# Kernel tuning notes

Hardware: AMD Instinct MI355X
Metric: run time of the kernel (lower is better)

The kernel has to match this reference:

```python
import jax, jax.numpy as jnp
import numpy as np

VOCAB_SIZE = 126
N_LABELS = VOCAB_SIZE + 2  # 128
START_IDX = N_LABELS - 2
STOP_IDX = N_LABELS - 1
NEG_INF = -10000.0


def setup_inputs() -> dict:
    key = jax.random.key(0)
    k1, k2, k3 = jax.random.split(key, 3)
    B, T = 512, 512
    logits = jax.random.normal(k1, (B, T, N_LABELS), dtype=jnp.float32)
    lens = jax.random.randint(k2, (B,), 1, T + 1, dtype=jnp.int64)
    transitions = jax.random.normal(k3, (N_LABELS, N_LABELS), dtype=jnp.float32)
    # CRF constraints from __init__: nothing transitions FROM start-as-target row,
    # nothing transitions INTO stop column (transitions[i, j] = score j -> i).
    transitions = transitions.at[START_IDX, :].set(NEG_INF)
    transitions = transitions.at[:, STOP_IDX].set(NEG_INF)
    return {"logits": logits, "lens": lens, "transitions": transitions}


def reference(logits, lens, transitions):
    """CRF forward algorithm (log partition function). Returns [B] norm."""
    B, T, n = logits.shape
    alpha0 = jnp.full((B, n), NEG_INF, dtype=logits.dtype).at[:, START_IDX].set(0.0)
    # mask[t, b] = 1 while t < lens[b] (matches c_lens > 0 per-step update)
    mask = (jnp.arange(T)[:, None] < lens[None, :]).astype(logits.dtype)  # [T, B]
    logits_t = jnp.transpose(logits, (1, 0, 2))  # [T, B, n]

    def step(alpha, inp):
        logit, m = inp  # [B, n], [B]
        # alpha_nxt[b, i] = logit[b, i] + logsumexp_j(trans[i, j] + alpha[b, j])
        alpha_nxt = jax.nn.logsumexp(transitions[None, :, :] + alpha[:, None, :], axis=2) + logit
        m = m[:, None]
        alpha = m * alpha_nxt + (1.0 - m) * alpha
        return alpha, None

    alpha, _ = jax.lax.scan(step, alpha0, (logits_t, mask))
    alpha = alpha + transitions[STOP_IDX][None, :]
    return jax.nn.logsumexp(alpha, axis=1)  # [B]
```

## Files before the change

### kernel.cpp

```cpp
#include <hip/hip_runtime.h>

#define NL 128
#define TT 512
#define NB 512
#define START_IDX 126
#define STOP_IDX 127

typedef __attribute__((ext_vector_type(8))) short bf16x8;
typedef __attribute__((ext_vector_type(4))) float f32x4;
typedef __attribute__((ext_vector_type(4))) unsigned u32x4;

__device__ __forceinline__ short f2bf(float x) {
    union { float f; unsigned u; } v; v.f = x;
    unsigned r = (v.u + 0x7FFFu + ((v.u >> 16) & 1u)) >> 16;
    return (short)r;
}

__device__ __forceinline__ unsigned cvt_pk_bf16(float lo, float hi) {
    unsigned r;
    asm("v_cvt_pk_bf16_f32 %0, %1, %2" : "=v"(r) : "v"(lo), "v"(hi));
    return r;
}

#define BAR() do {                                                            \
    asm volatile("s_waitcnt lgkmcnt(0)" ::: "memory");                        \
    __builtin_amdgcn_s_barrier();                                             \
} while (0)

#define MFMA16(A_, B_, C_) __builtin_amdgcn_mfma_f32_16x16x32_bf16(A_, B_, C_, 0, 0, 0)

#define STEP(T_, PUB_, CONS_, EU_, EB_, RS_, RD_) do {                        \
    u32x4 bo_ = {bw0, bw1, bw2, bw3};                                         \
    bf16x8 bO_ = __builtin_bit_cast(bf16x8, bo_);                             \
    bf16x8 bA_ = __builtin_bit_cast(bf16x8, bvA);                             \
    bf16x8 bB_ = __builtin_bit_cast(bf16x8, bvB);                             \
    bf16x8 bC_ = __builtin_bit_cast(bf16x8, bvC);                             \
    f32x4 a0_ = {0.f,0.f,0.f,0.f}, a1_ = {0.f,0.f,0.f,0.f};                   \
    a0_ = MFMA16(afr[0][0], bO_, a0_);                                        \
    a1_ = MFMA16(afr[1][0], bO_, a1_);                                        \
    a0_ = MFMA16(afr[0][1], bA_, a0_);                                        \
    a1_ = MFMA16(afr[1][1], bA_, a1_);                                        \
    a0_ = MFMA16(afr[0][2], bB_, a0_);                                        \
    a1_ = MFMA16(afr[1][2], bB_, a1_);                                        \
    a0_ = MFMA16(afr[0][3], bC_, a0_);                                        \
    a1_ = MFMA16(afr[1][3], bC_, a1_);                                        \
    { int tp_ = (T_) + 3; if (tp_ > TT - 1) tp_ = TT - 1;                     \
      const float* lp_ = lsrc + (size_t)tp_ * NL;                             \
      RD_##A = *(const f32x4*)(lp_ + eo0);                                    \
      RD_##B = *(const f32x4*)(lp_ + eo1); }                                  \
    _Pragma("unroll")                                                         \
    for (int r_ = 0; r_ < 4; ++r_) {                                          \
        EB_##A[r_] = __expf(RS_##A[r_]);                                      \
        EB_##B[r_] = __expf(RS_##B[r_]);                                      \
    }                                                                         \
    float nv0_[4], nv1_[4];                                                   \
    _Pragma("unroll")                                                         \
    for (int r_ = 0; r_ < 4; ++r_) {                                          \
        nv0_[r_] = a0_[r_] * EU_##A[r_];                                      \
        nv1_[r_] = a1_[r_] * EU_##B[r_];                                      \
    }                                                                         \
    const bool live_ = (T_) < lenc;                                           \
    if (CONS_) {                                                              \
        float mx_ = fmaxf(fmaxf(smax[0][c], smax[1][c]),                      \
                          fmaxf(smax[2][c], smax[3][c]));                     \
        const unsigned eb_ = (__float_as_uint(mx_) >> 23) & 0xFFu;            \
        const float sc_ = __uint_as_float(((253u - eb_) & 0xFFu) << 23);      \
        _Pragma("unroll")                                                     \
        for (int r_ = 0; r_ < 4; ++r_) { nv0_[r_] *= sc_; nv1_[r_] *= sc_; }  \
        if (live_) cbi += (int)eb_ - 126;                                     \
    }                                                                         \
    if (PUB_) {                                                               \
        float lm_ = fmaxf(fmaxf(fmaxf(nv0_[0], nv0_[1]), fmaxf(nv0_[2], nv0_[3])), \
                          fmaxf(fmaxf(nv1_[0], nv1_[1]), fmaxf(nv1_[2], nv1_[3]))); \
        lm_ = fmaxf(lm_, __shfl_xor(lm_, 16));                                \
        lm_ = fmaxf(lm_, __shfl_xor(lm_, 32));                                \
        if (g == 0) smax[w][c] = lm_;                                         \
    }                                                                         \
    { const unsigned n0_ = cvt_pk_bf16(nv0_[0], nv0_[1]);                     \
      const unsigned n1_ = cvt_pk_bf16(nv0_[2], nv0_[3]);                     \
      const unsigned n2_ = cvt_pk_bf16(nv1_[0], nv1_[1]);                     \
      const unsigned n3_ = cvt_pk_bf16(nv1_[2], nv1_[3]);                     \
      bw0 = live_ ? n0_ : bw0;  bw1 = live_ ? n1_ : bw1;                      \
      bw2 = live_ ? n2_ : bw2;  bw3 = live_ ? n3_ : bw3; }                    \
    char* nb_ = sb[((T_) + 1) & 1];                                           \
    { u32x4 wv_ = {bw0, bw1, bw2, bw3};                                       \
      *(u32x4*)(nb_ + w * 1280 + slotOff) = wv_; }                            \
    BAR();                                                                    \
    bvA = *(const u32x4*)(nb_ + kA + slotOff);                                \
    bvB = *(const u32x4*)(nb_ + kB + slotOff);                                \
    bvC = *(const u32x4*)(nb_ + kC + slotOff);                                \
} while (0)

__global__ __launch_bounds__(256)
void crf_scan(const float* __restrict__ logits,
              const int* __restrict__ lens,
              const float* __restrict__ trans,
              float* __restrict__ out)
{
    const int b0   = blockIdx.x * 16;
    const int tid  = threadIdx.x;
    const int w    = tid >> 6;
    const int lane = tid & 63;
    const int c    = lane & 15;
    const int g    = lane >> 4;

    __shared__ __align__(16) char sb[2][4 * 16 * 80];
    __shared__ float smax[4][16];

    bf16x8 afr[2][4];
    #pragma unroll
    for (int mi = 0; mi < 2; ++mi) {
        const int M = w + 4 * mi;
        const float* rowp = trans + (M * 16 + c) * NL + 4 * g;
        #pragma unroll
        for (int pos = 0; pos < 4; ++pos) {
            const int kk = (w + pos) & 3;
            f32x4 lo4 = *(const f32x4*)(rowp + kk * 16);
            f32x4 hi4 = *(const f32x4*)(rowp + (kk + 4) * 16);
            bf16x8 a;
            #pragma unroll
            for (int j = 0; j < 4; ++j) {
                a[j]     = f2bf(__expf(lo4[j]));
                a[j + 4] = f2bf(__expf(hi4[j]));
            }
            afr[mi][pos] = a;
        }
    }

    int lenc = lens[b0 + c];
    lenc = lenc < 1 ? 1 : (lenc > TT ? TT : lenc);
    int gl = lenc;
    #pragma unroll
    for (int d = 1; d < 16; d <<= 1) { int o = __shfl_xor(gl, d); gl = gl > o ? gl : o; }
    const int glen = __builtin_amdgcn_readfirstlane(gl);

    const int slotOff = c * 80 + g * 16;
    const int kA = ((w + 1) & 3) * 1280;
    const int kB = ((w + 2) & 3) * 1280;
    const int kC = ((w + 3) & 3) * 1280;

    unsigned bw0 = 0u, bw1 = 0u, bw2 = 0u,
             bw3 = (w == 3 && g == 3) ? 0x00003F80u : 0u;
    { u32x4 z = {bw0, bw1, bw2, bw3};
      *(u32x4*)(sb[0] + w * 1280 + slotOff) = z; }
    BAR();
    u32x4 bvA = *(const u32x4*)(sb[0] + kA + slotOff);
    u32x4 bvB = *(const u32x4*)(sb[0] + kB + slotOff);
    u32x4 bvC = *(const u32x4*)(sb[0] + kC + slotOff);

    const float* lsrc = logits + (size_t)(b0 + c) * TT * NL;
    const int eo0 = w * 16 + 4 * g;
    const int eo1 = (w + 4) * 16 + 4 * g;

    f32x4 R0A, R0B, R1A, R1B, R2A, R2B, R3A, R3B;
    f32x4 E0A, E0B, E1A, E1B;
    R0A = *(const f32x4*)(lsrc + eo0);            R0B = *(const f32x4*)(lsrc + eo1);
    R1A = *(const f32x4*)(lsrc + NL + eo0);       R1B = *(const f32x4*)(lsrc + NL + eo1);
    R2A = *(const f32x4*)(lsrc + 2 * NL + eo0);   R2B = *(const f32x4*)(lsrc + 2 * NL + eo1);
    #pragma unroll
    for (int r = 0; r < 4; ++r) {
        E0A[r] = __expf(R0A[r]);  E0B[r] = __expf(R0B[r]);
    }

    int cbi = 0;
    int t = 0;
    const int tmain = glen & ~3;
    for (; t < tmain; t += 4) {
        STEP(t + 0, false, false, E0, E1, R1, R3);
        STEP(t + 1, false, false, E1, E0, R2, R0);
        STEP(t + 2, true,  false, E0, E1, R3, R1);
        STEP(t + 3, false, true,  E1, E0, R0, R2);
    }
    if (t < glen) { STEP(t, false, false, E0, E1, R1, R3); ++t; }
    if (t < glen) { STEP(t, false, false, E1, E0, R2, R0); ++t; }
    if (t < glen) { STEP(t, true,  false, E0, E1, R3, R1); ++t; }

    if (w == 0) {
        float s = 0.f;
        const float* stopr = trans + STOP_IDX * NL + 4 * g;
        u32x4 grp[4];
        grp[0] = (u32x4){bw0, bw1, bw2, bw3};
        grp[1] = bvA; grp[2] = bvB; grp[3] = bvC;
        #pragma unroll
        for (int kk = 0; kk < 4; ++kk) {
            f32x4 t0 = *(const f32x4*)(stopr + kk * 16);
            f32x4 t1 = *(const f32x4*)(stopr + (kk + 4) * 16);
            #pragma unroll
            for (int i = 0; i < 2; ++i) {
                const unsigned wd = grp[kk][i];
                s += __uint_as_float(wd << 16)         * __expf(t0[2 * i]);
                s += __uint_as_float(wd & 0xFFFF0000u) * __expf(t0[2 * i + 1]);
            }
            #pragma unroll
            for (int i = 2; i < 4; ++i) {
                const unsigned wd = grp[kk][i];
                s += __uint_as_float(wd << 16)         * __expf(t1[2 * (i - 2)]);
                s += __uint_as_float(wd & 0xFFFF0000u) * __expf(t1[2 * (i - 2) + 1]);
            }
        }
        s += __shfl_xor(s, 16);
        s += __shfl_xor(s, 32);
        if (g == 0)
            out[b0 + c] = (float)cbi * 0.69314718055994531f + __logf(s);
    }
}

extern "C" void kernel_launch(void* const* d_in, const int* in_sizes, int n_in,
                              void* d_out, int out_size, void* d_ws, size_t ws_size,
                              hipStream_t stream) {
    const float* logits = (const float*)d_in[0];
    const int*   lens   = (const int*)d_in[1];
    const float* trans  = (const float*)d_in[2];
    float*       outp   = (float*)d_out;
    crf_scan<<<NB / 16, 256, 0, stream>>>(logits, lens, trans, outp);
}
```

Baseline: 150.6 us.

## Interleave two independent batch groups per block to hide scan-step latency

Each block now processes two 16-sequence groups (32 sequences) with duplicated register state, shared-memory buffers and max slots. The two groups' steps are interleaved so that one barrier per step serves both chains, and the MFMA and exp latency of one chain can overlap the other. The grid is halved to 16 blocks, so fewer CUs are in use. Each block also runs to the longest length among 32 sequences instead of 16, and register pressure roughly doubles.

```diff
diff --git a/kernel.cpp b/kernel.cpp
--- a/kernel.cpp
+++ b/kernel.cpp
@@ -29,83 +29,123 @@
 
 #define MFMA16(A_, B_, C_) __builtin_amdgcn_mfma_f32_16x16x32_bf16(A_, B_, C_, 0, 0, 0)
 
-#define STEP(T_, PUB_, CONS_, EU_, EB_, RS_, RD_) do {                        \
-    u32x4 bo_ = {bw0, bw1, bw2, bw3};                                         \
+#define STEP_PRE(P, PI_, T_, PUB_, CONS_, EU_, EB_, RS_, RD_) do {            \
+    u32x4 bo_ = {P##_bw0, P##_bw1, P##_bw2, P##_bw3};                         \
     bf16x8 bO_ = __builtin_bit_cast(bf16x8, bo_);                             \
-    bf16x8 bA_ = __builtin_bit_cast(bf16x8, bvA);                             \
-    bf16x8 bB_ = __builtin_bit_cast(bf16x8, bvB);                             \
-    bf16x8 bC_ = __builtin_bit_cast(bf16x8, bvC);                             \
+    bf16x8 bA_ = __builtin_bit_cast(bf16x8, P##_bvA);                         \
+    bf16x8 bB_ = __builtin_bit_cast(bf16x8, P##_bvB);                         \
+    bf16x8 bC_ = __builtin_bit_cast(bf16x8, P##_bvC);                         \
     f32x4 a0_ = {0.f,0.f,0.f,0.f}, a1_ = {0.f,0.f,0.f,0.f};                   \
-    a0_ = MFMA16(afr[0][0], bO_, a0_);                                        \
-    a1_ = MFMA16(afr[1][0], bO_, a1_);                                        \
-    a0_ = MFMA16(afr[0][1], bA_, a0_);                                        \
-    a1_ = MFMA16(afr[1][1], bA_, a1_);                                        \
-    a0_ = MFMA16(afr[0][2], bB_, a0_);                                        \
-    a1_ = MFMA16(afr[1][2], bB_, a1_);                                        \
-    a0_ = MFMA16(afr[0][3], bC_, a0_);                                        \
-    a1_ = MFMA16(afr[1][3], bC_, a1_);                                        \
+    a0_ = MFMA16(afr[0][0], bO_, a0_);  a1_ = MFMA16(afr[1][0], bO_, a1_);    \
+    a0_ = MFMA16(afr[0][1], bA_, a0_);  a1_ = MFMA16(afr[1][1], bA_, a1_);    \
+    a0_ = MFMA16(afr[0][2], bB_, a0_);  a1_ = MFMA16(afr[1][2], bB_, a1_);    \
+    a0_ = MFMA16(afr[0][3], bC_, a0_);  a1_ = MFMA16(afr[1][3], bC_, a1_);    \
     { int tp_ = (T_) + 3; if (tp_ > TT - 1) tp_ = TT - 1;                     \
-      const float* lp_ = lsrc + (size_t)tp_ * NL;                             \
-      RD_##A = *(const f32x4*)(lp_ + eo0);                                    \
-      RD_##B = *(const f32x4*)(lp_ + eo1); }                                  \
+      const float* lp_ = P##_lsrc + (size_t)tp_ * NL;                         \
+      P##_##RD_##X = *(const f32x4*)(lp_ + eo0);                              \
+      P##_##RD_##Y = *(const f32x4*)(lp_ + eo1); }                            \
     _Pragma("unroll")                                                         \
     for (int r_ = 0; r_ < 4; ++r_) {                                          \
-        EB_##A[r_] = __expf(RS_##A[r_]);                                      \
-        EB_##B[r_] = __expf(RS_##B[r_]);                                      \
+        P##_##EB_##X[r_] = __expf(P##_##RS_##X[r_]);                          \
+        P##_##EB_##Y[r_] = __expf(P##_##RS_##Y[r_]);                          \
     }                                                                         \
     float nv0_[4], nv1_[4];                                                   \
     _Pragma("unroll")                                                         \
     for (int r_ = 0; r_ < 4; ++r_) {                                          \
-        nv0_[r_] = a0_[r_] * EU_##A[r_];                                      \
-        nv1_[r_] = a1_[r_] * EU_##B[r_];                                      \
-    }                                                                         \
-    const bool live_ = (T_) < lenc;                                           \
+        nv0_[r_] = a0_[r_] * P##_##EU_##X[r_];                                \
+        nv1_[r_] = a1_[r_] * P##_##EU_##Y[r_];                                \
+    }                                                                         \
+    const bool live_ = (T_) < P##_lenc;                                       \
     if (CONS_) {                                                              \
-        float mx_ = fmaxf(fmaxf(smax[0][c], smax[1][c]),                      \
-                          fmaxf(smax[2][c], smax[3][c]));                     \
+        float mx_ = fmaxf(fmaxf(sm##P[0][c], sm##P[1][c]),                    \
+                          fmaxf(sm##P[2][c], sm##P[3][c]));                   \
         const unsigned eb_ = (__float_as_uint(mx_) >> 23) & 0xFFu;            \
         const float sc_ = __uint_as_float(((253u - eb_) & 0xFFu) << 23);      \
         _Pragma("unroll")                                                     \
         for (int r_ = 0; r_ < 4; ++r_) { nv0_[r_] *= sc_; nv1_[r_] *= sc_; }  \
-        if (live_) cbi += (int)eb_ - 126;                                     \
+        if (live_) P##_cbi += (int)eb_ - 126;                                 \
     }                                                                         \
     if (PUB_) {                                                               \
         float lm_ = fmaxf(fmaxf(fmaxf(nv0_[0], nv0_[1]), fmaxf(nv0_[2], nv0_[3])), \
                           fmaxf(fmaxf(nv1_[0], nv1_[1]), fmaxf(nv1_[2], nv1_[3]))); \
         lm_ = fmaxf(lm_, __shfl_xor(lm_, 16));                                \
         lm_ = fmaxf(lm_, __shfl_xor(lm_, 32));                                \
-        if (g == 0) smax[w][c] = lm_;                                         \
+        if (g == 0) sm##P[w][c] = lm_;                                        \
     }                                                                         \
     { const unsigned n0_ = cvt_pk_bf16(nv0_[0], nv0_[1]);                     \
       const unsigned n1_ = cvt_pk_bf16(nv0_[2], nv0_[3]);                     \
       const unsigned n2_ = cvt_pk_bf16(nv1_[0], nv1_[1]);                     \
       const unsigned n3_ = cvt_pk_bf16(nv1_[2], nv1_[3]);                     \
-      bw0 = live_ ? n0_ : bw0;  bw1 = live_ ? n1_ : bw1;                      \
-      bw2 = live_ ? n2_ : bw2;  bw3 = live_ ? n3_ : bw3; }                    \
-    char* nb_ = sb[((T_) + 1) & 1];                                           \
-    { u32x4 wv_ = {bw0, bw1, bw2, bw3};                                       \
-      *(u32x4*)(nb_ + w * 1280 + slotOff) = wv_; }                            \
+      P##_bw0 = live_ ? n0_ : P##_bw0;  P##_bw1 = live_ ? n1_ : P##_bw1;      \
+      P##_bw2 = live_ ? n2_ : P##_bw2;  P##_bw3 = live_ ? n3_ : P##_bw3; }    \
+    { u32x4 wv_ = {P##_bw0, P##_bw1, P##_bw2, P##_bw3};                       \
+      *(u32x4*)(&sb[PI_][((T_) + 1) & 1][0] + w * 1280 + slotOff) = wv_; }    \
+} while (0)
+
+#define STEP_POST(P, PI_, T_) do {                                            \
+    const char* nb_ = &sb[PI_][((T_) + 1) & 1][0];                            \
+    P##_bvA = *(const u32x4*)(nb_ + kA + slotOff);                            \
+    P##_bvB = *(const u32x4*)(nb_ + kB + slotOff);                            \
+    P##_bvC = *(const u32x4*)(nb_ + kC + slotOff);                            \
+} while (0)
+
+#define ROUND(T_, PUB_, CONS_, EU_, EB_, RS_, RD_) do {                       \
+    STEP_PRE(A, 0, T_, PUB_, CONS_, EU_, EB_, RS_, RD_);                      \
+    STEP_PRE(B, 1, T_, PUB_, CONS_, EU_, EB_, RS_, RD_);                      \
     BAR();                                                                    \
-    bvA = *(const u32x4*)(nb_ + kA + slotOff);                                \
-    bvB = *(const u32x4*)(nb_ + kB + slotOff);                                \
-    bvC = *(const u32x4*)(nb_ + kC + slotOff);                                \
-} while (0)
-
-__global__ __launch_bounds__(256)
+    STEP_POST(A, 0, T_);                                                      \
+    STEP_POST(B, 1, T_);                                                      \
+} while (0)
+
+#define EPILOG(P, BB_) do {                                                   \
+    float s = 0.f;                                                            \
+    const float* stopr = trans + STOP_IDX * NL + 4 * g;                       \
+    _Pragma("unroll")                                                         \
+    for (int pos = 0; pos < 4; ++pos) {                                       \
+        const int kk = (w + pos) & 3;                                         \
+        u32x4 gv;                                                             \
+        if (pos == 0)      gv = (u32x4){P##_bw0, P##_bw1, P##_bw2, P##_bw3};  \
+        else if (pos == 1) gv = P##_bvA;                                      \
+        else if (pos == 2) gv = P##_bvB;                                      \
+        else               gv = P##_bvC;                                      \
+        f32x4 t0 = *(const f32x4*)(stopr + kk * 16);                          \
+        f32x4 t1 = *(const f32x4*)(stopr + (kk + 4) * 16);                    \
+        _Pragma("unroll")                                                     \
+        for (int i = 0; i < 2; ++i) {                                         \
+            const unsigned wd = gv[i];                                        \
+            s += __uint_as_float(wd << 16)         * __expf(t0[2 * i]);       \
+            s += __uint_as_float(wd & 0xFFFF0000u) * __expf(t0[2 * i + 1]);   \
+        }                                                                     \
+        _Pragma("unroll")                                                     \
+        for (int i = 2; i < 4; ++i) {                                         \
+            const unsigned wd = gv[i];                                        \
+            s += __uint_as_float(wd << 16)         * __expf(t1[2 * (i - 2)]); \
+            s += __uint_as_float(wd & 0xFFFF0000u) * __expf(t1[2 * (i - 2) + 1]); \
+        }                                                                     \
+    }                                                                         \
+    s += __shfl_xor(s, 16);                                                   \
+    s += __shfl_xor(s, 32);                                                   \
+    if (g == 0)                                                               \
+        out[(BB_) + c] = (float)P##_cbi * 0.69314718055994531f + __logf(s);   \
+} while (0)
+
+__global__ __launch_bounds__(256, 1)
 void crf_scan(const float* __restrict__ logits,
               const int* __restrict__ lens,
               const float* __restrict__ trans,
               float* __restrict__ out)
 {
-    const int b0   = blockIdx.x * 16;
+    const int b0A  = blockIdx.x * 32;
+    const int b0B  = b0A + 16;
     const int tid  = threadIdx.x;
     const int w    = tid >> 6;
     const int lane = tid & 63;
     const int c    = lane & 15;
     const int g    = lane >> 4;
 
-    __shared__ __align__(16) char sb[2][4 * 16 * 80];
-    __shared__ float smax[4][16];
+    __shared__ __align__(16) char sb[2][2][4 * 16 * 80];
+    __shared__ float smA[4][16];
+    __shared__ float smB[4][16];
 
     bf16x8 afr[2][4];
     #pragma unroll
@@ -127,9 +167,11 @@
         }
     }
 
-    int lenc = lens[b0 + c];
-    lenc = lenc < 1 ? 1 : (lenc > TT ? TT : lenc);
-    int gl = lenc;
+    int A_lenc = lens[b0A + c];
+    A_lenc = A_lenc < 1 ? 1 : (A_lenc > TT ? TT : A_lenc);
+    int B_lenc = lens[b0B + c];
+    B_lenc = B_lenc < 1 ? 1 : (B_lenc > TT ? TT : B_lenc);
+    int gl = A_lenc > B_lenc ? A_lenc : B_lenc;
     #pragma unroll
     for (int d = 1; d < 16; d <<= 1) { int o = __shfl_xor(gl, d); gl = gl > o ? gl : o; }
     const int glen = __builtin_amdgcn_readfirstlane(gl);
@@ -139,70 +181,56 @@
     const int kB = ((w + 2) & 3) * 1280;
     const int kC = ((w + 3) & 3) * 1280;
 
-    unsigned bw0 = 0u, bw1 = 0u, bw2 = 0u,
-             bw3 = (w == 3 && g == 3) ? 0x00003F80u : 0u;
-    { u32x4 z = {bw0, bw1, bw2, bw3};
-      *(u32x4*)(sb[0] + w * 1280 + slotOff) = z; }
+    unsigned A_bw0 = 0u, A_bw1 = 0u, A_bw2 = 0u,
+             A_bw3 = (w == 3 && g == 3) ? 0x00003F80u : 0u;
+    unsigned B_bw0 = 0u, B_bw1 = 0u, B_bw2 = 0u, B_bw3 = A_bw3;
+    { u32x4 z = {A_bw0, A_bw1, A_bw2, A_bw3};
+      *(u32x4*)(&sb[0][0][0] + w * 1280 + slotOff) = z;
+      *(u32x4*)(&sb[1][0][0] + w * 1280 + slotOff) = z; }
     BAR();
-    u32x4 bvA = *(const u32x4*)(sb[0] + kA + slotOff);
-    u32x4 bvB = *(const u32x4*)(sb[0] + kB + slotOff);
-    u32x4 bvC = *(const u32x4*)(sb[0] + kC + slotOff);
-
-    const float* lsrc = logits + (size_t)(b0 + c) * TT * NL;
+    u32x4 A_bvA = *(const u32x4*)(&sb[0][0][0] + kA + slotOff);
+    u32x4 A_bvB = *(const u32x4*)(&sb[0][0][0] + kB + slotOff);
+    u32x4 A_bvC = *(const u32x4*)(&sb[0][0][0] + kC + slotOff);
+    u32x4 B_bvA = *(const u32x4*)(&sb[1][0][0] + kA + slotOff);
+    u32x4 B_bvB = *(const u32x4*)(&sb[1][0][0] + kB + slotOff);
+    u32x4 B_bvC = *(const u32x4*)(&sb[1][0][0] + kC + slotOff);
+
+    const float* A_lsrc = logits + (size_t)(b0A + c) * TT * NL;
+    const float* B_lsrc = logits + (size_t)(b0B + c) * TT * NL;
     const int eo0 = w * 16 + 4 * g;
     const int eo1 = (w + 4) * 16 + 4 * g;
 
-    f32x4 R0A, R0B, R1A, R1B, R2A, R2B, R3A, R3B;
-    f32x4 E0A, E0B, E1A, E1B;
-    R0A = *(const f32x4*)(lsrc + eo0);            R0B = *(const f32x4*)(lsrc + eo1);
-    R1A = *(const f32x4*)(lsrc + NL + eo0);       R1B = *(const f32x4*)(lsrc + NL + eo1);
-    R2A = *(const f32x4*)(lsrc + 2 * NL + eo0);   R2B = *(const f32x4*)(lsrc + 2 * NL + eo1);
+    f32x4 A_R0X, A_R0Y, A_R1X, A_R1Y, A_R2X, A_R2Y, A_R3X, A_R3Y;
+    f32x4 A_E0X, A_E0Y, A_E1X, A_E1Y;
+    f32x4 B_R0X, B_R0Y, B_R1X, B_R1Y, B_R2X, B_R2Y, B_R3X, B_R3Y;
+    f32x4 B_E0X, B_E0Y, B_E1X, B_E1Y;
+    A_R0X = *(const f32x4*)(A_lsrc + eo0);          A_R0Y = *(const f32x4*)(A_lsrc + eo1);
+    A_R1X = *(const f32x4*)(A_lsrc + NL + eo0);     A_R1Y = *(const f32x4*)(A_lsrc + NL + eo1);
+    A_R2X = *(const f32x4*)(A_lsrc + 2 * NL + eo0); A_R2Y = *(const f32x4*)(A_lsrc + 2 * NL + eo1);
+    B_R0X = *(const f32x4*)(B_lsrc + eo0);          B_R0Y = *(const f32x4*)(B_lsrc + eo1);
+    B_R1X = *(const f32x4*)(B_lsrc + NL + eo0);     B_R1Y = *(const f32x4*)(B_lsrc + NL + eo1);
+    B_R2X = *(const f32x4*)(B_lsrc + 2 * NL + eo0); B_R2Y = *(const f32x4*)(B_lsrc + 2 * NL + eo1);
     #pragma unroll
     for (int r = 0; r < 4; ++r) {
-        E0A[r] = __expf(R0A[r]);  E0B[r] = __expf(R0B[r]);
+        A_E0X[r] = __expf(A_R0X[r]);  A_E0Y[r] = __expf(A_R0Y[r]);
+        B_E0X[r] = __expf(B_R0X[r]);  B_E0Y[r] = __expf(B_R0Y[r]);
     }
 
-    int cbi = 0;
+    int A_cbi = 0, B_cbi = 0;
     int t = 0;
     const int tmain = glen & ~3;
     for (; t < tmain; t += 4) {
-        STEP(t + 0, false, false, E0, E1, R1, R3);
-        STEP(t + 1, false, false, E1, E0, R2, R0);
-        STEP(t + 2, true,  false, E0, E1, R3, R1);
-        STEP(t + 3, false, true,  E1, E0, R0, R2);
+        ROUND(t + 0, false, false, E0, E1, R1, R3);
+        ROUND(t + 1, false, false, E1, E0, R2, R0);
+        ROUND(t + 2, true,  false, E0, E1, R3, R1);
+        ROUND(t + 3, false, true,  E1, E0, R0, R2);
     }
-    if (t < glen) { STEP(t, false, false, E0, E1, R1, R3); ++t; }
-    if (t < glen) { STEP(t, false, false, E1, E0, R2, R0); ++t; }
-    if (t < glen) { STEP(t, true,  false, E0, E1, R3, R1); ++t; }
-
-    if (w == 0) {
-        float s = 0.f;
-        const float* stopr = trans + STOP_IDX * NL + 4 * g;
-        u32x4 grp[4];
-        grp[0] = (u32x4){bw0, bw1, bw2, bw3};
-        grp[1] = bvA; grp[2] = bvB; grp[3] = bvC;
-        #pragma unroll
-        for (int kk = 0; kk < 4; ++kk) {
-            f32x4 t0 = *(const f32x4*)(stopr + kk * 16);
-            f32x4 t1 = *(const f32x4*)(stopr + (kk + 4) * 16);
-            #pragma unroll
-            for (int i = 0; i < 2; ++i) {
-                const unsigned wd = grp[kk][i];
-                s += __uint_as_float(wd << 16)         * __expf(t0[2 * i]);
-                s += __uint_as_float(wd & 0xFFFF0000u) * __expf(t0[2 * i + 1]);
-            }
-            #pragma unroll
-            for (int i = 2; i < 4; ++i) {
-                const unsigned wd = grp[kk][i];
-                s += __uint_as_float(wd << 16)         * __expf(t1[2 * (i - 2)]);
-                s += __uint_as_float(wd & 0xFFFF0000u) * __expf(t1[2 * (i - 2) + 1]);
-            }
-        }
-        s += __shfl_xor(s, 16);
-        s += __shfl_xor(s, 32);
-        if (g == 0)
-            out[b0 + c] = (float)cbi * 0.69314718055994531f + __logf(s);
-    }
+    if (t < glen) { ROUND(t, false, false, E0, E1, R1, R3); ++t; }
+    if (t < glen) { ROUND(t, false, false, E1, E0, R2, R0); ++t; }
+    if (t < glen) { ROUND(t, true,  false, E0, E1, R3, R1); ++t; }
+
+    if (w == 0)      EPILOG(A, b0A);
+    else if (w == 1) EPILOG(B, b0B);
 }
 
 extern "C" void kernel_launch(void* const* d_in, const int* in_sizes, int n_in,
@@ -212,5 +240,5 @@
     const int*   lens   = (const int*)d_in[1];
     const float* trans  = (const float*)d_in[2];
     float*       outp   = (float*)d_out;
-    crf_scan<<<NB / 16, 256, 0, stream>>>(logits, lens, trans, outp);
-}
+    crf_scan<<<NB / 32, 256, 0, stream>>>(logits, lens, trans, outp);
+}
```

Result: slower. 251.9 us (+67.2%).

## Halve workgroup to two waves, each computing four output tiles per step

Applied to the files above, without the earlier changes.

Each block now runs 2 wavefronts instead of 4. Each wave computes 64 of the 128 output labels per step with 16 MFMAs, and the transition-matrix fragments held per wave double. The goal is to cut the per-step barrier and LDS exchange cost and the cross-wave max reduction in the serial recurrence. In exchange each wave does twice the MFMA and exp work per step, carries more registers, and the grid still has only 32 blocks, so per-step latency may grow.

```diff
diff --git a/kernel.cpp b/kernel.cpp
--- a/kernel.cpp
+++ b/kernel.cpp
@@ -30,68 +30,87 @@
 #define MFMA16(A_, B_, C_) __builtin_amdgcn_mfma_f32_16x16x32_bf16(A_, B_, C_, 0, 0, 0)
 
 #define STEP(T_, PUB_, CONS_, EU_, EB_, RS_, RD_) do {                        \
-    u32x4 bo_ = {bw0, bw1, bw2, bw3};                                         \
-    bf16x8 bO_ = __builtin_bit_cast(bf16x8, bo_);                             \
-    bf16x8 bA_ = __builtin_bit_cast(bf16x8, bvA);                             \
-    bf16x8 bB_ = __builtin_bit_cast(bf16x8, bvB);                             \
-    bf16x8 bC_ = __builtin_bit_cast(bf16x8, bvC);                             \
+    u32x4 bp_ = {bwP0, bwP1, bwP2, bwP3};                                     \
+    u32x4 bq_ = {bwQ0, bwQ1, bwQ2, bwQ3};                                     \
+    bf16x8 bP_ = __builtin_bit_cast(bf16x8, bp_);                             \
+    bf16x8 bQ_ = __builtin_bit_cast(bf16x8, bq_);                             \
+    bf16x8 bX_ = __builtin_bit_cast(bf16x8, bvX);                             \
+    bf16x8 bY_ = __builtin_bit_cast(bf16x8, bvY);                             \
     f32x4 a0_ = {0.f,0.f,0.f,0.f}, a1_ = {0.f,0.f,0.f,0.f};                   \
-    a0_ = MFMA16(afr[0][0], bO_, a0_);                                        \
-    a1_ = MFMA16(afr[1][0], bO_, a1_);                                        \
-    a0_ = MFMA16(afr[0][1], bA_, a0_);                                        \
-    a1_ = MFMA16(afr[1][1], bA_, a1_);                                        \
-    a0_ = MFMA16(afr[0][2], bB_, a0_);                                        \
-    a1_ = MFMA16(afr[1][2], bB_, a1_);                                        \
-    a0_ = MFMA16(afr[0][3], bC_, a0_);                                        \
-    a1_ = MFMA16(afr[1][3], bC_, a1_);                                        \
+    f32x4 a2_ = {0.f,0.f,0.f,0.f}, a3_ = {0.f,0.f,0.f,0.f};                   \
+    a0_ = MFMA16(afr[0][0], bP_, a0_);  a1_ = MFMA16(afr[1][0], bP_, a1_);    \
+    a2_ = MFMA16(afr[2][0], bP_, a2_);  a3_ = MFMA16(afr[3][0], bP_, a3_);    \
+    a0_ = MFMA16(afr[0][1], bQ_, a0_);  a1_ = MFMA16(afr[1][1], bQ_, a1_);    \
+    a2_ = MFMA16(afr[2][1], bQ_, a2_);  a3_ = MFMA16(afr[3][1], bQ_, a3_);    \
+    a0_ = MFMA16(afr[0][2], bX_, a0_);  a1_ = MFMA16(afr[1][2], bX_, a1_);    \
+    a2_ = MFMA16(afr[2][2], bX_, a2_);  a3_ = MFMA16(afr[3][2], bX_, a3_);    \
+    a0_ = MFMA16(afr[0][3], bY_, a0_);  a1_ = MFMA16(afr[1][3], bY_, a1_);    \
+    a2_ = MFMA16(afr[2][3], bY_, a2_);  a3_ = MFMA16(afr[3][3], bY_, a3_);    \
     { int tp_ = (T_) + 3; if (tp_ > TT - 1) tp_ = TT - 1;                     \
       const float* lp_ = lsrc + (size_t)tp_ * NL;                             \
-      RD_##A = *(const f32x4*)(lp_ + eo0);                                    \
-      RD_##B = *(const f32x4*)(lp_ + eo1); }                                  \
+      RD_##A = *(const f32x4*)(lp_ + eoA);                                    \
+      RD_##B = *(const f32x4*)(lp_ + eoB);                                    \
+      RD_##C = *(const f32x4*)(lp_ + eoC);                                    \
+      RD_##D = *(const f32x4*)(lp_ + eoD); }                                  \
     _Pragma("unroll")                                                         \
     for (int r_ = 0; r_ < 4; ++r_) {                                          \
         EB_##A[r_] = __expf(RS_##A[r_]);                                      \
         EB_##B[r_] = __expf(RS_##B[r_]);                                      \
-    }                                                                         \
-    float nv0_[4], nv1_[4];                                                   \
+        EB_##C[r_] = __expf(RS_##C[r_]);                                      \
+        EB_##D[r_] = __expf(RS_##D[r_]);                                      \
+    }                                                                         \
+    float nv0_[4], nv1_[4], nv2_[4], nv3_[4];                                 \
     _Pragma("unroll")                                                         \
     for (int r_ = 0; r_ < 4; ++r_) {                                          \
         nv0_[r_] = a0_[r_] * EU_##A[r_];                                      \
         nv1_[r_] = a1_[r_] * EU_##B[r_];                                      \
+        nv2_[r_] = a2_[r_] * EU_##C[r_];                                      \
+        nv3_[r_] = a3_[r_] * EU_##D[r_];                                      \
     }                                                                         \
     const bool live_ = (T_) < lenc;                                           \
     if (CONS_) {                                                              \
-        float mx_ = fmaxf(fmaxf(smax[0][c], smax[1][c]),                      \
-                          fmaxf(smax[2][c], smax[3][c]));                     \
+        float mx_ = fmaxf(smax[0][c], smax[1][c]);                            \
         const unsigned eb_ = (__float_as_uint(mx_) >> 23) & 0xFFu;            \
         const float sc_ = __uint_as_float(((253u - eb_) & 0xFFu) << 23);      \
         _Pragma("unroll")                                                     \
-        for (int r_ = 0; r_ < 4; ++r_) { nv0_[r_] *= sc_; nv1_[r_] *= sc_; }  \
+        for (int r_ = 0; r_ < 4; ++r_) {                                      \
+            nv0_[r_] *= sc_; nv1_[r_] *= sc_;                                 \
+            nv2_[r_] *= sc_; nv3_[r_] *= sc_;                                 \
+        }                                                                     \
         if (live_) cbi += (int)eb_ - 126;                                     \
     }                                                                         \
     if (PUB_) {                                                               \
         float lm_ = fmaxf(fmaxf(fmaxf(nv0_[0], nv0_[1]), fmaxf(nv0_[2], nv0_[3])), \
                           fmaxf(fmaxf(nv1_[0], nv1_[1]), fmaxf(nv1_[2], nv1_[3]))); \
+        lm_ = fmaxf(lm_, fmaxf(fmaxf(nv2_[0], nv2_[1]), fmaxf(nv2_[2], nv2_[3]))); \
+        lm_ = fmaxf(lm_, fmaxf(fmaxf(nv3_[0], nv3_[1]), fmaxf(nv3_[2], nv3_[3]))); \
         lm_ = fmaxf(lm_, __shfl_xor(lm_, 16));                                \
         lm_ = fmaxf(lm_, __shfl_xor(lm_, 32));                                \
         if (g == 0) smax[w][c] = lm_;                                         \
     }                                                                         \
-    { const unsigned n0_ = cvt_pk_bf16(nv0_[0], nv0_[1]);                     \
-      const unsigned n1_ = cvt_pk_bf16(nv0_[2], nv0_[3]);                     \
-      const unsigned n2_ = cvt_pk_bf16(nv1_[0], nv1_[1]);                     \
-      const unsigned n3_ = cvt_pk_bf16(nv1_[2], nv1_[3]);                     \
-      bw0 = live_ ? n0_ : bw0;  bw1 = live_ ? n1_ : bw1;                      \
-      bw2 = live_ ? n2_ : bw2;  bw3 = live_ ? n3_ : bw3; }                    \
+    { const unsigned p0_ = cvt_pk_bf16(nv0_[0], nv0_[1]);                     \
+      const unsigned p1_ = cvt_pk_bf16(nv0_[2], nv0_[3]);                     \
+      const unsigned p2_ = cvt_pk_bf16(nv2_[0], nv2_[1]);                     \
+      const unsigned p3_ = cvt_pk_bf16(nv2_[2], nv2_[3]);                     \
+      const unsigned q0_ = cvt_pk_bf16(nv1_[0], nv1_[1]);                     \
+      const unsigned q1_ = cvt_pk_bf16(nv1_[2], nv1_[3]);                     \
+      const unsigned q2_ = cvt_pk_bf16(nv3_[0], nv3_[1]);                     \
+      const unsigned q3_ = cvt_pk_bf16(nv3_[2], nv3_[3]);                     \
+      bwP0 = live_ ? p0_ : bwP0;  bwP1 = live_ ? p1_ : bwP1;                  \
+      bwP2 = live_ ? p2_ : bwP2;  bwP3 = live_ ? p3_ : bwP3;                  \
+      bwQ0 = live_ ? q0_ : bwQ0;  bwQ1 = live_ ? q1_ : bwQ1;                  \
+      bwQ2 = live_ ? q2_ : bwQ2;  bwQ3 = live_ ? q3_ : bwQ3; }                \
     char* nb_ = sb[((T_) + 1) & 1];                                           \
-    { u32x4 wv_ = {bw0, bw1, bw2, bw3};                                       \
-      *(u32x4*)(nb_ + w * 1280 + slotOff) = wv_; }                            \
+    { u32x4 wp_ = {bwP0, bwP1, bwP2, bwP3};                                   \
+      u32x4 wq_ = {bwQ0, bwQ1, bwQ2, bwQ3};                                   \
+      *(u32x4*)(nb_ + kP + slotOff) = wp_;                                    \
+      *(u32x4*)(nb_ + kQ + slotOff) = wq_; }                                  \
     BAR();                                                                    \
-    bvA = *(const u32x4*)(nb_ + kA + slotOff);                                \
-    bvB = *(const u32x4*)(nb_ + kB + slotOff);                                \
-    bvC = *(const u32x4*)(nb_ + kC + slotOff);                                \
+    bvX = *(const u32x4*)(nb_ + kX + slotOff);                                \
+    bvY = *(const u32x4*)(nb_ + kY + slotOff);                                \
 } while (0)
 
-__global__ __launch_bounds__(256)
+__global__ __launch_bounds__(128, 1)
 void crf_scan(const float* __restrict__ logits,
               const int* __restrict__ lens,
               const float* __restrict__ trans,
@@ -105,16 +124,21 @@
     const int g    = lane >> 4;
 
     __shared__ __align__(16) char sb[2][4 * 16 * 80];
-    __shared__ float smax[4][16];
-
-    bf16x8 afr[2][4];
+    __shared__ float smax[2][16];
+
+    const int kk0 = w;
+    const int kk1 = (w + 2) & 3;
+    const int kk2 = (w + 1) & 3;
+    const int kk3 = (w + 3) & 3;
+    bf16x8 afr[4][4];
     #pragma unroll
-    for (int mi = 0; mi < 2; ++mi) {
-        const int M = w + 4 * mi;
+    for (int mi = 0; mi < 4; ++mi) {
+        const int M = w + 2 * mi;
         const float* rowp = trans + (M * 16 + c) * NL + 4 * g;
+        const int kks[4] = {kk0, kk1, kk2, kk3};
         #pragma unroll
         for (int pos = 0; pos < 4; ++pos) {
-            const int kk = (w + pos) & 3;
+            const int kk = kks[pos];
             f32x4 lo4 = *(const f32x4*)(rowp + kk * 16);
             f32x4 hi4 = *(const f32x4*)(rowp + (kk + 4) * 16);
             bf16x8 a;
@@ -135,31 +159,41 @@
     const int glen = __builtin_amdgcn_readfirstlane(gl);
 
     const int slotOff = c * 80 + g * 16;
-    const int kA = ((w + 1) & 3) * 1280;
-    const int kB = ((w + 2) & 3) * 1280;
-    const int kC = ((w + 3) & 3) * 1280;
-
-    unsigned bw0 = 0u, bw1 = 0u, bw2 = 0u,
-             bw3 = (w == 3 && g == 3) ? 0x00003F80u : 0u;
-    { u32x4 z = {bw0, bw1, bw2, bw3};
-      *(u32x4*)(sb[0] + w * 1280 + slotOff) = z; }
+    const int kP = kk0 * 1280;
+    const int kQ = kk1 * 1280;
+    const int kX = kk2 * 1280;
+    const int kY = kk3 * 1280;
+
+    unsigned bwP0 = 0u, bwP1 = 0u, bwP2 = 0u, bwP3 = 0u;
+    unsigned bwQ0 = 0u, bwQ1 = 0u, bwQ2 = 0u,
+             bwQ3 = (w == 1 && g == 3) ? 0x00003F80u : 0u;
+    { u32x4 zp = {bwP0, bwP1, bwP2, bwP3};
+      u32x4 zq = {bwQ0, bwQ1, bwQ2, bwQ3};
+      *(u32x4*)(sb[0] + kP + slotOff) = zp;
+      *(u32x4*)(sb[0] + kQ + slotOff) = zq; }
     BAR();
-    u32x4 bvA = *(const u32x4*)(sb[0] + kA + slotOff);
-    u32x4 bvB = *(const u32x4*)(sb[0] + kB + slotOff);
-    u32x4 bvC = *(const u32x4*)(sb[0] + kC + slotOff);
+    u32x4 bvX = *(const u32x4*)(sb[0] + kX + slotOff);
+    u32x4 bvY = *(const u32x4*)(sb[0] + kY + slotOff);
 
     const float* lsrc = logits + (size_t)(b0 + c) * TT * NL;
-    const int eo0 = w * 16 + 4 * g;
-    const int eo1 = (w + 4) * 16 + 4 * g;
-
-    f32x4 R0A, R0B, R1A, R1B, R2A, R2B, R3A, R3B;
-    f32x4 E0A, E0B, E1A, E1B;
-    R0A = *(const f32x4*)(lsrc + eo0);            R0B = *(const f32x4*)(lsrc + eo1);
-    R1A = *(const f32x4*)(lsrc + NL + eo0);       R1B = *(const f32x4*)(lsrc + NL + eo1);
-    R2A = *(const f32x4*)(lsrc + 2 * NL + eo0);   R2B = *(const f32x4*)(lsrc + 2 * NL + eo1);
+    const int eoA = (w + 0) * 16 + 4 * g;
+    const int eoB = (w + 2) * 16 + 4 * g;
+    const int eoC = (w + 4) * 16 + 4 * g;
+    const int eoD = (w + 6) * 16 + 4 * g;
+
+    f32x4 R0A, R0B, R0C, R0D, R1A, R1B, R1C, R1D;
+    f32x4 R2A, R2B, R2C, R2D, R3A, R3B, R3C, R3D;
+    f32x4 E0A, E0B, E0C, E0D, E1A, E1B, E1C, E1D;
+    R0A = *(const f32x4*)(lsrc + eoA);          R0B = *(const f32x4*)(lsrc + eoB);
+    R0C = *(const f32x4*)(lsrc + eoC);          R0D = *(const f32x4*)(lsrc + eoD);
+    R1A = *(const f32x4*)(lsrc + NL + eoA);     R1B = *(const f32x4*)(lsrc + NL + eoB);
+    R1C = *(const f32x4*)(lsrc + NL + eoC);     R1D = *(const f32x4*)(lsrc + NL + eoD);
+    R2A = *(const f32x4*)(lsrc + 2*NL + eoA);   R2B = *(const f32x4*)(lsrc + 2*NL + eoB);
+    R2C = *(const f32x4*)(lsrc + 2*NL + eoC);   R2D = *(const f32x4*)(lsrc + 2*NL + eoD);
     #pragma unroll
     for (int r = 0; r < 4; ++r) {
         E0A[r] = __expf(R0A[r]);  E0B[r] = __expf(R0B[r]);
+        E0C[r] = __expf(R0C[r]);  E0D[r] = __expf(R0D[r]);
     }
 
     int cbi = 0;
@@ -178,22 +212,24 @@
     if (w == 0) {
         float s = 0.f;
         const float* stopr = trans + STOP_IDX * NL + 4 * g;
-        u32x4 grp[4];
-        grp[0] = (u32x4){bw0, bw1, bw2, bw3};
-        grp[1] = bvA; grp[2] = bvB; grp[3] = bvC;
+        u32x4 gvk[4];
+        gvk[0] = (u32x4){bwP0, bwP1, bwP2, bwP3};
+        gvk[2] = (u32x4){bwQ0, bwQ1, bwQ2, bwQ3};
+        gvk[1] = bvX;
+        gvk[3] = bvY;
         #pragma unroll
         for (int kk = 0; kk < 4; ++kk) {
             f32x4 t0 = *(const f32x4*)(stopr + kk * 16);
             f32x4 t1 = *(const f32x4*)(stopr + (kk + 4) * 16);
             #pragma unroll
             for (int i = 0; i < 2; ++i) {
-                const unsigned wd = grp[kk][i];
+                const unsigned wd = gvk[kk][i];
                 s += __uint_as_float(wd << 16)         * __expf(t0[2 * i]);
                 s += __uint_as_float(wd & 0xFFFF0000u) * __expf(t0[2 * i + 1]);
             }
             #pragma unroll
             for (int i = 2; i < 4; ++i) {
-                const unsigned wd = grp[kk][i];
+                const unsigned wd = gvk[kk][i];
                 s += __uint_as_float(wd << 16)         * __expf(t1[2 * (i - 2)]);
                 s += __uint_as_float(wd & 0xFFFF0000u) * __expf(t1[2 * (i - 2) + 1]);
             }
@@ -212,5 +248,5 @@
     const int*   lens   = (const int*)d_in[1];
     const float* trans  = (const float*)d_in[2];
     float*       outp   = (float*)d_out;
-    crf_scan<<<NB / 16, 256, 0, stream>>>(logits, lens, trans, outp);
-}
+    crf_scan<<<NB / 16, 128, 0, stream>>>(logits, lens, trans, outp);
+}
```

Result: slower. 202.3 us (+34.3%).

## Pack two independent 16-sequence groups into each 512-thread block

Applied to the files above, without the earlier changes.

Each workgroup now runs two independent 16-batch CRF scans in 8 waves instead of one in 4. Shared buffers and max scratch are duplicated per group, and the grid is halved. This concentrates work on fewer CUs, possibly improving per-CU utilisation or scheduling. In exchange, the block-wide barriers now synchronise both groups, and the loop trip count becomes the maximum length over 32 sequences instead of 16.

```diff
diff --git a/kernel.cpp b/kernel.cpp
--- a/kernel.cpp
+++ b/kernel.cpp
@@ -61,8 +61,8 @@
     }                                                                         \
     const bool live_ = (T_) < lenc;                                           \
     if (CONS_) {                                                              \
-        float mx_ = fmaxf(fmaxf(smax[0][c], smax[1][c]),                      \
-                          fmaxf(smax[2][c], smax[3][c]));                     \
+        float mx_ = fmaxf(fmaxf(smx[0][c], smx[1][c]),                        \
+                          fmaxf(smx[2][c], smx[3][c]));                       \
         const unsigned eb_ = (__float_as_uint(mx_) >> 23) & 0xFFu;            \
         const float sc_ = __uint_as_float(((253u - eb_) & 0xFFu) << 23);      \
         _Pragma("unroll")                                                     \
@@ -74,7 +74,7 @@
                           fmaxf(fmaxf(nv1_[0], nv1_[1]), fmaxf(nv1_[2], nv1_[3]))); \
         lm_ = fmaxf(lm_, __shfl_xor(lm_, 16));                                \
         lm_ = fmaxf(lm_, __shfl_xor(lm_, 32));                                \
-        if (g == 0) smax[w][c] = lm_;                                         \
+        if (g == 0) smx[w4][c] = lm_;                                         \
     }                                                                         \
     { const unsigned n0_ = cvt_pk_bf16(nv0_[0], nv0_[1]);                     \
       const unsigned n1_ = cvt_pk_bf16(nv0_[2], nv0_[3]);                     \
@@ -82,39 +82,47 @@
       const unsigned n3_ = cvt_pk_bf16(nv1_[2], nv1_[3]);                     \
       bw0 = live_ ? n0_ : bw0;  bw1 = live_ ? n1_ : bw1;                      \
       bw2 = live_ ? n2_ : bw2;  bw3 = live_ ? n3_ : bw3; }                    \
-    char* nb_ = sb[((T_) + 1) & 1];                                           \
+    char* nb_ = ((T_) & 1) ? sbuf0 : sbuf1;              \
     { u32x4 wv_ = {bw0, bw1, bw2, bw3};                                       \
-      *(u32x4*)(nb_ + w * 1280 + slotOff) = wv_; }                            \
+      *(u32x4*)(nb_ + w4 * 1280 + slotOff) = wv_; }                           \
     BAR();                                                                    \
     bvA = *(const u32x4*)(nb_ + kA + slotOff);                                \
     bvB = *(const u32x4*)(nb_ + kB + slotOff);                                \
     bvC = *(const u32x4*)(nb_ + kC + slotOff);                                \
 } while (0)
 
-__global__ __launch_bounds__(256)
+__global__ __launch_bounds__(512, 2)
 void crf_scan(const float* __restrict__ logits,
               const int* __restrict__ lens,
               const float* __restrict__ trans,
               float* __restrict__ out)
 {
-    const int b0   = blockIdx.x * 16;
     const int tid  = threadIdx.x;
     const int w    = tid >> 6;
+    const int p    = w >> 2;
+    const int w4   = w & 3;
     const int lane = tid & 63;
     const int c    = lane & 15;
     const int g    = lane >> 4;
 
-    __shared__ __align__(16) char sb[2][4 * 16 * 80];
-    __shared__ float smax[4][16];
+    const int base = blockIdx.x * 32;
+    const int b0   = base + p * 16;
+
+    __shared__ __align__(16) char sb[2][2][4 * 16 * 80];
+    __shared__ float smax[2][4][16];
+
+    char* sbuf0 = &sb[p][0][0];
+    char* sbuf1 = &sb[p][1][0];
+    float (*smx)[16] = smax[p];
 
     bf16x8 afr[2][4];
     #pragma unroll
     for (int mi = 0; mi < 2; ++mi) {
-        const int M = w + 4 * mi;
+        const int M = w4 + 4 * mi;
         const float* rowp = trans + (M * 16 + c) * NL + 4 * g;
         #pragma unroll
         for (int pos = 0; pos < 4; ++pos) {
-            const int kk = (w + pos) & 3;
+            const int kk = (w4 + pos) & 3;
             f32x4 lo4 = *(const f32x4*)(rowp + kk * 16);
             f32x4 hi4 = *(const f32x4*)(rowp + (kk + 4) * 16);
             bf16x8 a;
@@ -129,28 +137,31 @@
 
     int lenc = lens[b0 + c];
     lenc = lenc < 1 ? 1 : (lenc > TT ? TT : lenc);
-    int gl = lenc;
+    int lA = lens[base + c];
+    int lB = lens[base + 16 + c];
+    int gl = lA > lB ? lA : lB;
+    gl = gl < 1 ? 1 : (gl > TT ? TT : gl);
     #pragma unroll
     for (int d = 1; d < 16; d <<= 1) { int o = __shfl_xor(gl, d); gl = gl > o ? gl : o; }
     const int glen = __builtin_amdgcn_readfirstlane(gl);
 
     const int slotOff = c * 80 + g * 16;
-    const int kA = ((w + 1) & 3) * 1280;
-    const int kB = ((w + 2) & 3) * 1280;
-    const int kC = ((w + 3) & 3) * 1280;
+    const int kA = ((w4 + 1) & 3) * 1280;
+    const int kB = ((w4 + 2) & 3) * 1280;
+    const int kC = ((w4 + 3) & 3) * 1280;
 
     unsigned bw0 = 0u, bw1 = 0u, bw2 = 0u,
-             bw3 = (w == 3 && g == 3) ? 0x00003F80u : 0u;
+             bw3 = (w4 == 3 && g == 3) ? 0x00003F80u : 0u;
     { u32x4 z = {bw0, bw1, bw2, bw3};
-      *(u32x4*)(sb[0] + w * 1280 + slotOff) = z; }
+      *(u32x4*)(sbuf0 + w4 * 1280 + slotOff) = z; }
     BAR();
-    u32x4 bvA = *(const u32x4*)(sb[0] + kA + slotOff);
-    u32x4 bvB = *(const u32x4*)(sb[0] + kB + slotOff);
-    u32x4 bvC = *(const u32x4*)(sb[0] + kC + slotOff);
+    u32x4 bvA = *(const u32x4*)(sbuf0 + kA + slotOff);
+    u32x4 bvB = *(const u32x4*)(sbuf0 + kB + slotOff);
+    u32x4 bvC = *(const u32x4*)(sbuf0 + kC + slotOff);
 
     const float* lsrc = logits + (size_t)(b0 + c) * TT * NL;
-    const int eo0 = w * 16 + 4 * g;
-    const int eo1 = (w + 4) * 16 + 4 * g;
+    const int eo0 = w4 * 16 + 4 * g;
+    const int eo1 = (w4 + 4) * 16 + 4 * g;
 
     f32x4 R0A, R0B, R1A, R1B, R2A, R2B, R3A, R3B;
     f32x4 E0A, E0B, E1A, E1B;
@@ -175,7 +186,7 @@
     if (t < glen) { STEP(t, false, false, E1, E0, R2, R0); ++t; }
     if (t < glen) { STEP(t, true,  false, E0, E1, R3, R1); ++t; }
 
-    if (w == 0) {
+    if (w4 == 0) {
         float s = 0.f;
         const float* stopr = trans + STOP_IDX * NL + 4 * g;
         u32x4 grp[4];
@@ -212,5 +223,5 @@
     const int*   lens   = (const int*)d_in[1];
     const float* trans  = (const float*)d_in[2];
     float*       outp   = (float*)d_out;
-    crf_scan<<<NB / 16, 256, 0, stream>>>(logits, lens, trans, outp);
-}
+    crf_scan<<<NB / 32, 512, 0, stream>>>(logits, lens, trans, outp);
+}
```

New measurement: 239.1 us. 1.59x slower.
